# Kernel optimization log

Hardware: AMD Instinct MI355X
Metric: run time of the kernel (lower is better)

## Reference

```python
import jax, jax.numpy as jnp
import numpy as np

N, C = 50000, 91
K_PRE = 1000            # pre-NMS top-k candidates (fixed shape for jit)
DET_PER_IMG = 100
SCORE_THRESH = 0.05
NMS_THRESH = 0.5
MIN_SIZE = 0.01
LOG_SCALE_CLAMP = float(np.log(1000.0 / 16.0))  # torchvision BoxCoder clamp
BBOX_W = (10.0, 10.0, 5.0, 5.0)


def setup_inputs() -> dict:
    key = jax.random.key(0)
    k1, k2, k3, k4, k5, k6 = jax.random.split(key, 6)
    class_logits = jax.random.normal(k1, (N, C), jnp.float32) * 2.0
    box_regression = jax.random.normal(k2, (N, C * 4), jnp.float32) * 0.5
    x1 = jax.random.uniform(k3, (N,), jnp.float32) * 1200.0
    y1 = jax.random.uniform(k4, (N,), jnp.float32) * 700.0
    w = jax.random.uniform(k5, (N,), jnp.float32) * 150.0 + 4.0
    h = jax.random.uniform(k6, (N,), jnp.float32) * 150.0 + 4.0
    proposals = jnp.stack([x1, y1, x1 + w, y1 + h], axis=1)
    return {"class_logits": class_logits, "box_regression": box_regression,
            "proposals": proposals, "image_h": 800, "image_w": 1333}


def _decode(rel, props):
    # torchvision BoxCoder.decode_single with weights (10,10,5,5)
    wx, wy, ww, wh = BBOX_W
    pw = props[:, 2] - props[:, 0]
    ph = props[:, 3] - props[:, 1]
    cx = props[:, 0] + 0.5 * pw
    cy = props[:, 1] + 0.5 * ph
    dx = rel[:, 0] / wx
    dy = rel[:, 1] / wy
    dw = jnp.minimum(rel[:, 2] / ww, LOG_SCALE_CLAMP)
    dh = jnp.minimum(rel[:, 3] / wh, LOG_SCALE_CLAMP)
    pcx = dx * pw + cx
    pcy = dy * ph + cy
    ppw = jnp.exp(dw) * pw
    pph = jnp.exp(dh) * ph
    return jnp.stack([pcx - 0.5 * ppw, pcy - 0.5 * pph,
                      pcx + 0.5 * ppw, pcy + 0.5 * pph], axis=1)


def _iou_matrix(b):
    # b: [K,4] -> [K,K] pairwise IoU
    area = jnp.maximum(b[:, 2] - b[:, 0], 0.0) * jnp.maximum(b[:, 3] - b[:, 1], 0.0)
    lt = jnp.maximum(b[:, None, :2], b[None, :, :2])
    rb = jnp.minimum(b[:, None, 2:], b[None, :, 2:])
    wh = jnp.maximum(rb - lt, 0.0)
    inter = wh[..., 0] * wh[..., 1]
    return inter / (area[:, None] + area[None, :] - inter + 1e-7)


def _postprocess(class_logits, box_regression, proposals, image_h, image_w):
    num_classes = class_logits.shape[-1]
    n = proposals.shape[0]
    props = jnp.broadcast_to(proposals[:, None, :], (n, num_classes, 4)).reshape(-1, 4)
    boxes = _decode(box_regression.reshape(-1, 4), props)       # [N*C, 4]
    # clip_boxes_to_image
    boxes = jnp.stack([
        jnp.clip(boxes[:, 0], 0.0, float(image_w)),
        jnp.clip(boxes[:, 1], 0.0, float(image_h)),
        jnp.clip(boxes[:, 2], 0.0, float(image_w)),
        jnp.clip(boxes[:, 3], 0.0, float(image_h)),
    ], axis=1)
    scores = jax.nn.softmax(class_logits, axis=-1)               # [N, C]
    # drop background class 0
    boxes = boxes.reshape(n, num_classes, 4)[:, 1:].reshape(-1, 4)    # [N*(C-1), 4]
    scores = scores[:, 1:].reshape(-1)                                # [N*(C-1)]
    labels = jnp.broadcast_to(jnp.arange(1, num_classes), (n, num_classes - 1)).reshape(-1)
    # score threshold + remove small boxes -> mask (fixed-shape)
    w = boxes[:, 2] - boxes[:, 0]
    h = boxes[:, 3] - boxes[:, 1]
    valid = (scores > SCORE_THRESH) & (w >= MIN_SIZE) & (h >= MIN_SIZE)
    masked_scores = jnp.where(valid, scores, -1.0)
    s_k, idx = jax.lax.top_k(masked_scores, K_PRE)               # pre-NMS candidates
    b_k = boxes[idx]
    l_k = labels[idx]
    keep0 = s_k > 0.0
    # batched NMS via per-class coordinate offset
    offset = l_k.astype(b_k.dtype) * float(image_w + image_h + 2)
    iou = _iou_matrix(b_k + offset[:, None])                     # [K,K]
    ar = jnp.arange(K_PRE)
    def body(i, keep):
        sup = keep[i] & (iou[i] > NMS_THRESH) & (ar > i)
        return keep & ~sup
    keep = jax.lax.fori_loop(0, K_PRE, body, keep0)
    final_scores = jnp.where(keep, s_k, -1.0)
    s_out, j = jax.lax.top_k(final_scores, DET_PER_IMG)
    ok = s_out > 0.0
    boxes_out = jnp.where(ok[:, None], b_k[j], 0.0)
    scores_out = jnp.where(ok, s_out, 0.0)
    labels_out = jnp.where(ok, l_k[j], 0)
    return boxes_out, scores_out, labels_out


def reference(class_logits, box_regression, proposals, image_h, image_w):
    return _postprocess(class_logits, box_regression, proposals, image_h, image_w)
```

## Files before the change

### kernel.cpp

```cpp
#include <hip/hip_runtime.h>
#include <cstdint>

#define NROWS 50000
#define NCLS  91
#define KPRE  1000
#define NDET  100
#define CAP   4096
#define BIN_OFF 62770u
#define LOGCLAMP 4.135166556742356f
#define P1BLK 3125
#define R2BLK 49
#define NFINE 256
#define NU4   6250
#define CPS   3136
#define CP4   3528
#define GCHUNK 128

constexpr size_t OFF_CNT     = 0;
constexpr size_t OFF_ROWMAX  = 64;
constexpr size_t OFF_COMPACT = 100096;
constexpr size_t OFF_SSCORE  = 132864;
constexpr size_t OFF_SGIDX   = 136960;
constexpr size_t OFF_SLABEL  = 141056;
constexpr size_t OFF_BRAW    = 145152;
constexpr size_t OFF_BNMS    = 161536;
constexpr size_t OFF_MASK    = 177920;
constexpr size_t OFF_CPART   = 305920;

__device__ __forceinline__ bool decode_box(int row, int c,
    const float* __restrict__ regr, const float* __restrict__ props,
    float W, float H, float4& b) {
  const float4 rr = *reinterpret_cast<const float4*>(regr + (size_t)row * (NCLS * 4) + c * 4);
  const float4 pp = *reinterpret_cast<const float4*>(props + (size_t)row * 4);
  float pw = pp.z - pp.x, ph = pp.w - pp.y;
  float cx = pp.x + 0.5f * pw, cy = pp.y + 0.5f * ph;
  float dx = rr.x / 10.0f, dy = rr.y / 10.0f;
  float dw = fminf(rr.z / 5.0f, LOGCLAMP);
  float dh = fminf(rr.w / 5.0f, LOGCLAMP);
  float pcx = dx * pw + cx, pcy = dy * ph + cy;
  float ppw = expf(dw) * pw, pph = expf(dh) * ph;
  float x1 = fminf(fmaxf(pcx - 0.5f * ppw, 0.f), W);
  float y1 = fminf(fmaxf(pcy - 0.5f * pph, 0.f), H);
  float x2 = fminf(fmaxf(pcx + 0.5f * ppw, 0.f), W);
  float y2 = fminf(fmaxf(pcy + 0.5f * pph, 0.f), H);
  b = make_float4(x1, y1, x2, y2);
  return (x2 - x1 >= 0.01f) && (y2 - y1 >= 0.01f);
}

__device__ __forceinline__ bool decode_box_v(const float4& rr, const float4& pp,
                                             float W, float H, float4& b) {
  float pw = pp.z - pp.x, ph = pp.w - pp.y;
  float cx = pp.x + 0.5f * pw, cy = pp.y + 0.5f * ph;
  float dx = rr.x / 10.0f, dy = rr.y / 10.0f;
  float dw = fminf(rr.z / 5.0f, LOGCLAMP);
  float dh = fminf(rr.w / 5.0f, LOGCLAMP);
  float pcx = dx * pw + cx, pcy = dy * ph + cy;
  float ppw = expf(dw) * pw, pph = expf(dh) * ph;
  float x1 = fminf(fmaxf(pcx - 0.5f * ppw, 0.f), W);
  float y1 = fminf(fmaxf(pcy - 0.5f * pph, 0.f), H);
  float x2 = fminf(fmaxf(pcx + 0.5f * ppw, 0.f), W);
  float y2 = fminf(fmaxf(pcy + 0.5f * pph, 0.f), H);
  b = make_float4(x1, y1, x2, y2);
  return (x2 - x1 >= 0.01f) && (y2 - y1 >= 0.01f);
}

__global__ __launch_bounds__(256)
void pass1_kernel(const float* __restrict__ logits,
                  const float* __restrict__ regr,
                  const float* __restrict__ props,
                  const int* __restrict__ p_imh,
                  const int* __restrict__ p_imw,
                  uint16_t* __restrict__ rowmax,
                  uint16_t* __restrict__ cpart,
                  uint32_t* __restrict__ cnt) {
  __shared__ uint32_t lds9[9];
  const int t = threadIdx.x;
  if (blockIdx.x == 0 && t == 0) cnt[1] = 0;
  if (t < 9) lds9[t] = 0;
  __syncthreads();

  const int gt  = blockIdx.x * 256 + t;
  const int row = gt >> 4;
  const int sub = gt & 15;
  const float* lr = logits + (size_t)row * NCLS;
  const float4 pp = *reinterpret_cast<const float4*>(props + (size_t)row * 4);
  const float W = (float)(*p_imw), H = (float)(*p_imh);

  float x[6];
  #pragma unroll
  for (int j = 0; j < 6; ++j) {
    int c = sub + 16 * j;
    x[j] = (c < NCLS) ? lr[c] : -INFINITY;
  }
  float m = x[0];
  #pragma unroll
  for (int j = 1; j < 6; ++j) m = fmaxf(m, x[j]);
  m = fmaxf(m, __shfl_xor(m, 1));
  m = fmaxf(m, __shfl_xor(m, 2));
  m = fmaxf(m, __shfl_xor(m, 4));
  m = fmaxf(m, __shfl_xor(m, 8));
  float e[6]; float s = 0.f;
  #pragma unroll
  for (int j = 0; j < 6; ++j) {
    e[j] = (sub + 16 * j < NCLS) ? expf(x[j] - m) : 0.f;
    s += e[j];
  }
  s += __shfl_xor(s, 1);
  s += __shfl_xor(s, 2);
  s += __shfl_xor(s, 4);
  s += __shfl_xor(s, 8);

  const float4* rr4 = reinterpret_cast<const float4*>(regr) + (size_t)row * NCLS;
  float score[6]; bool ok[6]; float4 rrv[6];
  #pragma unroll
  for (int j = 0; j < 6; ++j) {
    int c = sub + 16 * j;
    score[j] = e[j] / s;
    ok[j] = (c >= 1) && (c < NCLS) && (score[j] > 0.05f);
    rrv[j] = ok[j] ? rr4[c] : make_float4(0.f, 0.f, 0.f, 0.f);
  }
  int maxbin = 0;
  #pragma unroll
  for (int j = 0; j < 6; ++j) {
    if (ok[j]) {
      float4 b;
      if (decode_box_v(rrv[j], pp, W, H, b)) {
        uint32_t bin = (__float_as_uint(score[j]) >> 14) - BIN_OFF;
        if ((int)bin > maxbin) maxbin = (int)bin;
      }
    }
  }
  maxbin = max(maxbin, __shfl_xor(maxbin, 1));
  maxbin = max(maxbin, __shfl_xor(maxbin, 2));
  maxbin = max(maxbin, __shfl_xor(maxbin, 4));
  maxbin = max(maxbin, __shfl_xor(maxbin, 8));
  if (sub == 0) {
    rowmax[row] = (uint16_t)maxbin;
    if (maxbin > 0) atomicAdd(&lds9[maxbin >> 8], 1u);
  }
  __syncthreads();
  if (t < 9) cpart[(size_t)t * CPS + blockIdx.x] = (uint16_t)lds9[t];
  if (blockIdx.x < 9 && t < CPS - P1BLK)
    cpart[(size_t)blockIdx.x * CPS + P1BLK + t] = 0;
}

__global__ __launch_bounds__(1024)
void refine_kernel(const float* __restrict__ logits,
                   const float* __restrict__ regr,
                   const float* __restrict__ props,
                   const int* __restrict__ p_imh,
                   const int* __restrict__ p_imw,
                   const uint16_t* __restrict__ rowmax,
                   const uint16_t* __restrict__ cpart,
                   uint32_t* __restrict__ cnt,
                   unsigned long long* __restrict__ compact) {
  __shared__ uint32_t fine[NFINE + 1];
  __shared__ uint32_t lds9[9];
  __shared__ uint32_t s_cut;
  const int t = threadIdx.x;
  if (t < 9) lds9[t] = 0;
  if (t < NFINE + 1) fine[t] = 0;
  if (t == 0) s_cut = 0xFFFFFFFFu;
  __syncthreads();

  const uint4* cp4 = reinterpret_cast<const uint4*>(cpart);
  for (int k = t; k < CP4; k += 1024) {
    uint4 v = cp4[k];
    uint32_t ssum = (v.x & 0xffffu) + (v.x >> 16) + (v.y & 0xffffu) + (v.y >> 16) +
                    (v.z & 0xffffu) + (v.z >> 16) + (v.w & 0xffffu) + (v.w >> 16);
    if (ssum) atomicAdd(&lds9[k / 392], ssum);
  }
  __syncthreads();
  uint32_t sfx[10];
  sfx[9] = 0;
  #pragma unroll
  for (int q = 8; q >= 0; --q) sfx[q] = sfx[q + 1] + lds9[q];
  const uint32_t total = sfx[0];
  uint32_t cut;
  if (total == 0) {
    cut = 0xFFFFFFFFu;
  } else {
    const uint32_t target = total < (uint32_t)KPRE ? total : (uint32_t)KPRE;
    int Bc = 0;
    uint32_t S_hi = 0;
    #pragma unroll
    for (int q = 8; q >= 0; --q) {
      if (sfx[q] >= target && sfx[q + 1] < target) { Bc = q; S_hi = sfx[q + 1]; }
    }
    const uint4* r128 = reinterpret_cast<const uint4*>(rowmax);
    for (int k = t; k < NU4; k += 1024) {
      uint4 v = r128[k];
      #pragma unroll
      for (int w = 0; w < 4; ++w) {
        uint32_t u = (w == 0) ? v.x : (w == 1) ? v.y : (w == 2) ? v.z : v.w;
        uint32_t a = u & 0xffffu, b = u >> 16;
        if (a && (a >> 8) == (uint32_t)Bc) atomicAdd(&fine[a & 255u], 1u);
        if (b && (b >> 8) == (uint32_t)Bc) atomicAdd(&fine[b & 255u], 1u);
      }
    }
    __syncthreads();
    for (int off = 1; off < NFINE; off <<= 1) {
      uint32_t add = (t < NFINE && t + off < NFINE) ? fine[t + off] : 0;
      __syncthreads();
      if (t < NFINE) fine[t] += add;
      __syncthreads();
    }
    if (t < NFINE) {
      uint32_t hi = S_hi + fine[t];
      uint32_t hin = S_hi + ((t < NFINE - 1) ? fine[t + 1] : 0);
      if (hi >= target && hin < target) s_cut = ((uint32_t)Bc << 8) + (uint32_t)t;
    }
    __syncthreads();
    cut = s_cut;
  }

  const int lane = t & 63;
  const int g16 = lane >> 4;
  const int sub = lane & 15;
  const float W = (float)(*p_imw), H = (float)(*p_imh);
  const int base = blockIdx.x * 1024;
  const int myrow0 = base + t;
  bool qual = (myrow0 < NROWS) && ((uint32_t)rowmax[myrow0] >= cut);
  unsigned long long bm = __ballot(qual);
  if (!bm) return;
  const int waveBase = base + (t & ~63);
  while (bm) {
    int bsel[4];
    #pragma unroll
    for (int k = 0; k < 4; ++k) {
      bsel[k] = bm ? (__ffsll((unsigned long long)bm) - 1) : -1;
      if (bm) bm &= bm - 1;
    }
    const int myb = bsel[g16];
    const int row = waveBase + (myb >= 0 ? myb : 0);
    const float* lr = logits + (size_t)row * NCLS;
    float x[6];
    #pragma unroll
    for (int j = 0; j < 6; ++j) {
      int c = sub + 16 * j;
      x[j] = (c < NCLS) ? lr[c] : -INFINITY;
    }
    float m = x[0];
    #pragma unroll
    for (int j = 1; j < 6; ++j) m = fmaxf(m, x[j]);
    m = fmaxf(m, __shfl_xor(m, 1));
    m = fmaxf(m, __shfl_xor(m, 2));
    m = fmaxf(m, __shfl_xor(m, 4));
    m = fmaxf(m, __shfl_xor(m, 8));
    float e[6]; float s = 0.f;
    #pragma unroll
    for (int j = 0; j < 6; ++j) {
      e[j] = (sub + 16 * j < NCLS) ? expf(x[j] - m) : 0.f;
      s += e[j];
    }
    s += __shfl_xor(s, 1);
    s += __shfl_xor(s, 2);
    s += __shfl_xor(s, 4);
    s += __shfl_xor(s, 8);
    if (myb >= 0) {
      #pragma unroll
      for (int j = 0; j < 6; ++j) {
        int c = sub + 16 * j;
        if (c >= 1 && c < NCLS) {
          float score = e[j] / s;
          if (score > 0.05f) {
            float4 bb;
            if (decode_box(row, c, regr, props, W, H, bb)) {
              uint32_t bits = __float_as_uint(score);
              uint32_t bin = (bits >> 14) - BIN_OFF;
              if (bin >= cut) {
                uint32_t pos = atomicAdd(&cnt[1], 1u);
                if (pos < CAP) {
                  uint32_t gidx = (uint32_t)row * 90u + (uint32_t)(c - 1);
                  compact[pos] = ((unsigned long long)bits << 32) |
                                 (unsigned long long)(0xFFFFFFFFu - gidx);
                }
              }
            }
          }
        }
      }
    }
  }
}

__global__ __launch_bounds__(1024)
void sort_prep_kernel(const unsigned long long* __restrict__ compact,
                      const uint32_t* __restrict__ cnt,
                      const float* __restrict__ regr, const float* __restrict__ props,
                      const int* __restrict__ p_imh, const int* __restrict__ p_imw,
                      float* __restrict__ sel_score, uint32_t* __restrict__ sel_gidx,
                      int* __restrict__ slabel, float4* __restrict__ braw,
                      float4* __restrict__ bnms) {
  __shared__ unsigned long long arr[CAP];
  const int t = threadIdx.x;
  const uint32_t M = cnt[1] < (uint32_t)CAP ? cnt[1] : (uint32_t)CAP;
  int P = 1024;
  while (P < (int)M) P <<= 1;
  for (int i = t; i < P; i += 1024) arr[i] = (i < (int)M) ? compact[i] : 0ull;
  __syncthreads();
  for (int k = 2; k <= P; k <<= 1) {
    for (int j = k >> 1; j > 0; j >>= 1) {
      for (int i = t; i < P; i += 1024) {
        int l = i ^ j;
        if (l > i) {
          unsigned long long A = arr[i], B = arr[l];
          bool up = ((i & k) == 0);
          if (up ? (A > B) : (A < B)) { arr[i] = B; arr[l] = A; }
        }
      }
      __syncthreads();
    }
  }
  if (t < KPRE) {
    unsigned long long en = arr[P - 1 - t];
    float sc; uint32_t g;
    if (en) { sc = __uint_as_float((uint32_t)(en >> 32)); g = 0xFFFFFFFFu - (uint32_t)en; }
    else    { sc = -1.f; g = 0xFFFFFFFFu; }
    sel_score[t] = sc;
    sel_gidx[t] = g;
    if (sc > 0.f) {
      int row = (int)(g / 90u);
      int c   = (int)(g % 90u) + 1;
      float W = (float)(*p_imw), H = (float)(*p_imh);
      float4 b;
      decode_box(row, c, regr, props, W, H, b);
      braw[t] = b;
      float offv = (float)c * (float)(*p_imw + *p_imh + 2);
      bnms[t] = make_float4(b.x + offv, b.y + offv, b.z + offv, b.w + offv);
      slabel[t] = c;
    } else {
      braw[t] = make_float4(0, 0, 0, 0);
      bnms[t] = make_float4(0, 0, 0, 0);
      slabel[t] = 0;
    }
  }
}

__global__ __launch_bounds__(256)
void iou_kernel(const float4* __restrict__ bnms, unsigned long long* __restrict__ mask) {
  const int i = blockIdx.x;
  const int lane = threadIdx.x & 63;
  const int wv = threadIdx.x >> 6;
  const float4 bi = bnms[i];
  const float areai = fmaxf(bi.z - bi.x, 0.f) * fmaxf(bi.w - bi.y, 0.f);
  #pragma unroll
  for (int ww = 0; ww < 4; ++ww) {
    int wd = wv * 4 + ww;
    int j = wd * 64 + lane;
    bool bit = false;
    if (j < KPRE && j > i) {
      float4 bj = bnms[j];
      float areaj = fmaxf(bj.z - bj.x, 0.f) * fmaxf(bj.w - bj.y, 0.f);
      float ltx = fmaxf(bi.x, bj.x), lty = fmaxf(bi.y, bj.y);
      float rbx = fminf(bi.z, bj.z), rby = fminf(bi.w, bj.w);
      float iw = fmaxf(rbx - ltx, 0.f), ih = fmaxf(rby - lty, 0.f);
      float inter = iw * ih;
      float iou = inter / (areai + areaj - inter + 1e-7f);
      bit = iou > 0.5f;
    }
    unsigned long long mword = __ballot(bit);
    if (lane == 0) mask[(size_t)i * 16 + wd] = mword;
  }
}

__global__ __launch_bounds__(256)
void greedy_kernel(const unsigned long long* __restrict__ mask,
                   const float* __restrict__ sel_score,
                   const int* __restrict__ slabel,
                   const float4* __restrict__ braw,
                   float* __restrict__ out) {
  __shared__ ulonglong2 buf[2][GCHUNK * 8];
  __shared__ int kept[NDET];
  __shared__ int s_done;
  const int t = threadIdx.x;
  const int lane = t & 63;
  const int wv = t >> 6;
  const ulonglong2* gm2 = reinterpret_cast<const ulonglong2*>(mask);
  constexpr int NCHUNK = (KPRE + GCHUNK - 1) / GCHUNK;

  unsigned long long kw = 0ull;
  #pragma unroll
  for (int w = 0; w < 16; ++w) {
    int j = w * 64 + lane;
    bool b = (j < KPRE) && (sel_score[j] > 0.f);
    unsigned long long mword = __ballot(b);
    if (lane == w) kw = mword;
  }
  if (t == 0) s_done = 0;

  {
    int rows = (KPRE < GCHUNK) ? KPRE : GCHUNK;
    int n2 = rows * 8;
    for (int k = t; k < n2; k += 256) buf[0][k] = gm2[k];
  }
  __syncthreads();

  int kc = 0;
  for (int c = 0; c < NCHUNK; ++c) {
    if (wv > 0 && c + 1 < NCHUNK) {
      int rows = KPRE - (c + 1) * GCHUNK;
      if (rows > GCHUNK) rows = GCHUNK;
      int n2 = rows * 8;
      size_t gbase = (size_t)(c + 1) * GCHUNK * 8;
      for (int k = t - 64; k < n2; k += 192) buf[(c + 1) & 1][k] = gm2[gbase + k];
    }
    if (wv == 0) {
      const unsigned long long* bb =
          reinterpret_cast<const unsigned long long*>(buf[c & 1]);
      int rows = KPRE - c * GCHUNK;
      if (rows > GCHUNK) rows = GCHUNK;
      unsigned long long curm = (lane < 16) ? bb[lane] : 0ull;
      for (int r = 0; r < rows; ++r) {
        unsigned long long nxt =
            (lane < 16 && r + 1 < rows) ? bb[(r + 1) * 16 + lane] : 0ull;
        int i = c * GCHUNK + r;
        unsigned long long kwv = __shfl(kw, i >> 6);
        if ((kwv >> (i & 63)) & 1ull) {
          if (lane == 0) kept[kc] = i;
          kw &= ~curm;
          ++kc;
          if (kc >= NDET) { if (lane == 0) s_done = 1; break; }
        }
        curm = nxt;
      }
    }
    __syncthreads();
    if (s_done) break;
  }

  if (wv == 0) {
    for (int q = lane; q < NDET; q += 64) {
      if (q < kc) {
        int i = kept[q];
        float4 b = braw[i];
        out[q * 4 + 0] = b.x; out[q * 4 + 1] = b.y;
        out[q * 4 + 2] = b.z; out[q * 4 + 3] = b.w;
        out[4 * NDET + q] = sel_score[i];
        out[5 * NDET + q] = (float)slabel[i];
      } else {
        out[q * 4 + 0] = 0.f; out[q * 4 + 1] = 0.f;
        out[q * 4 + 2] = 0.f; out[q * 4 + 3] = 0.f;
        out[4 * NDET + q] = 0.f;
        out[5 * NDET + q] = 0.f;
      }
    }
  }
}

extern "C" void kernel_launch(void* const* d_in, const int* in_sizes, int n_in,
                              void* d_out, int out_size, void* d_ws, size_t ws_size,
                              hipStream_t stream) {
  const float* logits = (const float*)d_in[0];
  const float* regr   = (const float*)d_in[1];
  const float* props  = (const float*)d_in[2];
  const int*   p_imh  = (const int*)d_in[3];
  const int*   p_imw  = (const int*)d_in[4];
  float* out = (float*)d_out;

  uint8_t* ws = (uint8_t*)d_ws;
  uint32_t* cnt  = (uint32_t*)(ws + OFF_CNT);
  uint16_t* rowmax = (uint16_t*)(ws + OFF_ROWMAX);
  unsigned long long* compact = (unsigned long long*)(ws + OFF_COMPACT);
  float*    sel_score = (float*)(ws + OFF_SSCORE);
  uint32_t* sel_gidx  = (uint32_t*)(ws + OFF_SGIDX);
  int*      slabel    = (int*)(ws + OFF_SLABEL);
  float4*   braw      = (float4*)(ws + OFF_BRAW);
  float4*   bnms      = (float4*)(ws + OFF_BNMS);
  unsigned long long* mask = (unsigned long long*)(ws + OFF_MASK);
  uint16_t* cpart     = (uint16_t*)(ws + OFF_CPART);

  pass1_kernel<<<P1BLK, 256, 0, stream>>>(
      logits, regr, props, p_imh, p_imw, rowmax, cpart, cnt);
  refine_kernel<<<R2BLK, 1024, 0, stream>>>(
      logits, regr, props, p_imh, p_imw, rowmax, cpart, cnt, compact);
  sort_prep_kernel<<<1, 1024, 0, stream>>>(compact, cnt, regr, props, p_imh, p_imw,
                                           sel_score, sel_gidx, slabel, braw, bnms);
  iou_kernel<<<KPRE, 256, 0, stream>>>(bnms, mask);
  greedy_kernel<<<1, 256, 0, stream>>>(mask, sel_score, slabel, braw, out);
}
```

Before: 90.01 us.

## Fuse sort into refine and greedy NMS into IoU via last-block-done pattern

The single-block sort/prep kernel is folded into the refine kernel, and the greedy NMS kernel is folded into the IoU kernel. In each case an atomic counter elects the last finishing block, which then runs the serial stage. This cuts two kernel launches and their inter-kernel gaps from the five-launch pipeline. In exchange, refine blocks now reserve 32KB of shared memory for the sort array, which may lower occupancy, and correctness now depends on threadfence ordering.

Result: slower. 161.4 us (+79.4%).

```diff
diff --git a/kernel.cpp b/kernel.cpp
--- a/kernel.cpp
+++ b/kernel.cpp
@@ -75,7 +75,7 @@
                   uint32_t* __restrict__ cnt) {
   __shared__ uint32_t lds9[9];
   const int t = threadIdx.x;
-  if (blockIdx.x == 0 && t == 0) cnt[1] = 0;
+  if (blockIdx.x == 0 && t == 0) { cnt[1] = 0; cnt[2] = 0; cnt[3] = 0; }
   if (t < 9) lds9[t] = 0;
   __syncthreads();
 
@@ -153,10 +153,15 @@
                    const uint16_t* __restrict__ rowmax,
                    const uint16_t* __restrict__ cpart,
                    uint32_t* __restrict__ cnt,
-                   unsigned long long* __restrict__ compact) {
+                   unsigned long long* __restrict__ compact,
+                   float* __restrict__ sel_score, uint32_t* __restrict__ sel_gidx,
+                   int* __restrict__ slabel, float4* __restrict__ braw,
+                   float4* __restrict__ bnms) {
+  __shared__ unsigned long long arr[CAP];
   __shared__ uint32_t fine[NFINE + 1];
   __shared__ uint32_t lds9[9];
   __shared__ uint32_t s_cut;
+  __shared__ uint32_t s_prev;
   const int t = threadIdx.x;
   if (t < 9) lds9[t] = 0;
   if (t < NFINE + 1) fine[t] = 0;
@@ -214,66 +219,67 @@
     cut = s_cut;
   }
 
-  const int lane = t & 63;
-  const int g16 = lane >> 4;
-  const int sub = lane & 15;
-  const float W = (float)(*p_imw), H = (float)(*p_imh);
-  const int base = blockIdx.x * 1024;
-  const int myrow0 = base + t;
-  bool qual = (myrow0 < NROWS) && ((uint32_t)rowmax[myrow0] >= cut);
-  unsigned long long bm = __ballot(qual);
-  if (!bm) return;
-  const int waveBase = base + (t & ~63);
-  while (bm) {
-    int bsel[4];
-    #pragma unroll
-    for (int k = 0; k < 4; ++k) {
-      bsel[k] = bm ? (__ffsll((unsigned long long)bm) - 1) : -1;
-      if (bm) bm &= bm - 1;
-    }
-    const int myb = bsel[g16];
-    const int row = waveBase + (myb >= 0 ? myb : 0);
-    const float* lr = logits + (size_t)row * NCLS;
-    float x[6];
-    #pragma unroll
-    for (int j = 0; j < 6; ++j) {
-      int c = sub + 16 * j;
-      x[j] = (c < NCLS) ? lr[c] : -INFINITY;
-    }
-    float m = x[0];
-    #pragma unroll
-    for (int j = 1; j < 6; ++j) m = fmaxf(m, x[j]);
-    m = fmaxf(m, __shfl_xor(m, 1));
-    m = fmaxf(m, __shfl_xor(m, 2));
-    m = fmaxf(m, __shfl_xor(m, 4));
-    m = fmaxf(m, __shfl_xor(m, 8));
-    float e[6]; float s = 0.f;
-    #pragma unroll
-    for (int j = 0; j < 6; ++j) {
-      e[j] = (sub + 16 * j < NCLS) ? expf(x[j] - m) : 0.f;
-      s += e[j];
-    }
-    s += __shfl_xor(s, 1);
-    s += __shfl_xor(s, 2);
-    s += __shfl_xor(s, 4);
-    s += __shfl_xor(s, 8);
-    if (myb >= 0) {
+  {
+    const int lane = t & 63;
+    const int g16 = lane >> 4;
+    const int sub = lane & 15;
+    const float W = (float)(*p_imw), H = (float)(*p_imh);
+    const int base = blockIdx.x * 1024;
+    const int myrow0 = base + t;
+    bool qual = (myrow0 < NROWS) && ((uint32_t)rowmax[myrow0] >= cut);
+    unsigned long long bm = __ballot(qual);
+    const int waveBase = base + (t & ~63);
+    while (bm) {
+      int bsel[4];
+      #pragma unroll
+      for (int k = 0; k < 4; ++k) {
+        bsel[k] = bm ? (__ffsll((unsigned long long)bm) - 1) : -1;
+        if (bm) bm &= bm - 1;
+      }
+      const int myb = bsel[g16];
+      const int row = waveBase + (myb >= 0 ? myb : 0);
+      const float* lr = logits + (size_t)row * NCLS;
+      float x[6];
       #pragma unroll
       for (int j = 0; j < 6; ++j) {
         int c = sub + 16 * j;
-        if (c >= 1 && c < NCLS) {
-          float score = e[j] / s;
-          if (score > 0.05f) {
-            float4 bb;
-            if (decode_box(row, c, regr, props, W, H, bb)) {
-              uint32_t bits = __float_as_uint(score);
-              uint32_t bin = (bits >> 14) - BIN_OFF;
-              if (bin >= cut) {
-                uint32_t pos = atomicAdd(&cnt[1], 1u);
-                if (pos < CAP) {
-                  uint32_t gidx = (uint32_t)row * 90u + (uint32_t)(c - 1);
-                  compact[pos] = ((unsigned long long)bits << 32) |
-                                 (unsigned long long)(0xFFFFFFFFu - gidx);
+        x[j] = (c < NCLS) ? lr[c] : -INFINITY;
+      }
+      float m = x[0];
+      #pragma unroll
+      for (int j = 1; j < 6; ++j) m = fmaxf(m, x[j]);
+      m = fmaxf(m, __shfl_xor(m, 1));
+      m = fmaxf(m, __shfl_xor(m, 2));
+      m = fmaxf(m, __shfl_xor(m, 4));
+      m = fmaxf(m, __shfl_xor(m, 8));
+      float e[6]; float s = 0.f;
+      #pragma unroll
+      for (int j = 0; j < 6; ++j) {
+        e[j] = (sub + 16 * j < NCLS) ? expf(x[j] - m) : 0.f;
+        s += e[j];
+      }
+      s += __shfl_xor(s, 1);
+      s += __shfl_xor(s, 2);
+      s += __shfl_xor(s, 4);
+      s += __shfl_xor(s, 8);
+      if (myb >= 0) {
+        #pragma unroll
+        for (int j = 0; j < 6; ++j) {
+          int c = sub + 16 * j;
+          if (c >= 1 && c < NCLS) {
+            float score = e[j] / s;
+            if (score > 0.05f) {
+              float4 bb;
+              if (decode_box(row, c, regr, props, W, H, bb)) {
+                uint32_t bits = __float_as_uint(score);
+                uint32_t bin = (bits >> 14) - BIN_OFF;
+                if (bin >= cut) {
+                  uint32_t pos = atomicAdd(&cnt[1], 1u);
+                  if (pos < CAP) {
+                    uint32_t gidx = (uint32_t)row * 90u + (uint32_t)(c - 1);
+                    compact[pos] = ((unsigned long long)bits << 32) |
+                                   (unsigned long long)(0xFFFFFFFFu - gidx);
+                  }
                 }
               }
             }
@@ -282,18 +288,14 @@
       }
     }
   }
-}
-
-__global__ __launch_bounds__(1024)
-void sort_prep_kernel(const unsigned long long* __restrict__ compact,
-                      const uint32_t* __restrict__ cnt,
-                      const float* __restrict__ regr, const float* __restrict__ props,
-                      const int* __restrict__ p_imh, const int* __restrict__ p_imw,
-                      float* __restrict__ sel_score, uint32_t* __restrict__ sel_gidx,
-                      int* __restrict__ slabel, float4* __restrict__ braw,
-                      float4* __restrict__ bnms) {
-  __shared__ unsigned long long arr[CAP];
-  const int t = threadIdx.x;
+
+  __syncthreads();
+  __threadfence();
+  if (t == 0) s_prev = atomicAdd(&cnt[2], 1u);
+  __syncthreads();
+  if (s_prev != (uint32_t)(R2BLK - 1)) return;
+  __threadfence();
+
   const uint32_t M = cnt[1] < (uint32_t)CAP ? cnt[1] : (uint32_t)CAP;
   int P = 1024;
   while (P < (int)M) P <<= 1;
@@ -338,44 +340,50 @@
 }
 
 __global__ __launch_bounds__(256)
-void iou_kernel(const float4* __restrict__ bnms, unsigned long long* __restrict__ mask) {
-  const int i = blockIdx.x;
-  const int lane = threadIdx.x & 63;
-  const int wv = threadIdx.x >> 6;
-  const float4 bi = bnms[i];
-  const float areai = fmaxf(bi.z - bi.x, 0.f) * fmaxf(bi.w - bi.y, 0.f);
-  #pragma unroll
-  for (int ww = 0; ww < 4; ++ww) {
-    int wd = wv * 4 + ww;
-    int j = wd * 64 + lane;
-    bool bit = false;
-    if (j < KPRE && j > i) {
-      float4 bj = bnms[j];
-      float areaj = fmaxf(bj.z - bj.x, 0.f) * fmaxf(bj.w - bj.y, 0.f);
-      float ltx = fmaxf(bi.x, bj.x), lty = fmaxf(bi.y, bj.y);
-      float rbx = fminf(bi.z, bj.z), rby = fminf(bi.w, bj.w);
-      float iw = fmaxf(rbx - ltx, 0.f), ih = fmaxf(rby - lty, 0.f);
-      float inter = iw * ih;
-      float iou = inter / (areai + areaj - inter + 1e-7f);
-      bit = iou > 0.5f;
-    }
-    unsigned long long mword = __ballot(bit);
-    if (lane == 0) mask[(size_t)i * 16 + wd] = mword;
-  }
-}
-
-__global__ __launch_bounds__(256)
-void greedy_kernel(const unsigned long long* __restrict__ mask,
-                   const float* __restrict__ sel_score,
-                   const int* __restrict__ slabel,
-                   const float4* __restrict__ braw,
-                   float* __restrict__ out) {
+void iou_kernel(const float4* __restrict__ bnms, unsigned long long* __restrict__ mask,
+                const float* __restrict__ sel_score,
+                const int* __restrict__ slabel,
+                const float4* __restrict__ braw,
+                uint32_t* __restrict__ cnt,
+                float* __restrict__ out) {
   __shared__ ulonglong2 buf[2][GCHUNK * 8];
   __shared__ int kept[NDET];
   __shared__ int s_done;
+  __shared__ uint32_t s_prev;
+  const int i = blockIdx.x;
   const int t = threadIdx.x;
   const int lane = t & 63;
   const int wv = t >> 6;
+  {
+    const float4 bi = bnms[i];
+    const float areai = fmaxf(bi.z - bi.x, 0.f) * fmaxf(bi.w - bi.y, 0.f);
+    #pragma unroll
+    for (int ww = 0; ww < 4; ++ww) {
+      int wd = wv * 4 + ww;
+      int j = wd * 64 + lane;
+      bool bit = false;
+      if (j < KPRE && j > i) {
+        float4 bj = bnms[j];
+        float areaj = fmaxf(bj.z - bj.x, 0.f) * fmaxf(bj.w - bj.y, 0.f);
+        float ltx = fmaxf(bi.x, bj.x), lty = fmaxf(bi.y, bj.y);
+        float rbx = fminf(bi.z, bj.z), rby = fminf(bi.w, bj.w);
+        float iw = fmaxf(rbx - ltx, 0.f), ih = fmaxf(rby - lty, 0.f);
+        float inter = iw * ih;
+        float iou = inter / (areai + areaj - inter + 1e-7f);
+        bit = iou > 0.5f;
+      }
+      unsigned long long mword = __ballot(bit);
+      if (lane == 0) mask[(size_t)i * 16 + wd] = mword;
+    }
+  }
+
+  __syncthreads();
+  __threadfence();
+  if (t == 0) s_prev = atomicAdd(&cnt[3], 1u);
+  __syncthreads();
+  if (s_prev != (uint32_t)(KPRE - 1)) return;
+  __threadfence();
+
   const ulonglong2* gm2 = reinterpret_cast<const ulonglong2*>(mask);
   constexpr int NCHUNK = (KPRE + GCHUNK - 1) / GCHUNK;
 
@@ -414,10 +422,10 @@
       for (int r = 0; r < rows; ++r) {
         unsigned long long nxt =
             (lane < 16 && r + 1 < rows) ? bb[(r + 1) * 16 + lane] : 0ull;
-        int i = c * GCHUNK + r;
-        unsigned long long kwv = __shfl(kw, i >> 6);
-        if ((kwv >> (i & 63)) & 1ull) {
-          if (lane == 0) kept[kc] = i;
+        int ii = c * GCHUNK + r;
+        unsigned long long kwv = __shfl(kw, ii >> 6);
+        if ((kwv >> (ii & 63)) & 1ull) {
+          if (lane == 0) kept[kc] = ii;
           kw &= ~curm;
           ++kc;
           if (kc >= NDET) { if (lane == 0) s_done = 1; break; }
@@ -432,12 +440,12 @@
   if (wv == 0) {
     for (int q = lane; q < NDET; q += 64) {
       if (q < kc) {
-        int i = kept[q];
-        float4 b = braw[i];
+        int ii = kept[q];
+        float4 b = braw[ii];
         out[q * 4 + 0] = b.x; out[q * 4 + 1] = b.y;
         out[q * 4 + 2] = b.z; out[q * 4 + 3] = b.w;
-        out[4 * NDET + q] = sel_score[i];
-        out[5 * NDET + q] = (float)slabel[i];
+        out[4 * NDET + q] = sel_score[ii];
+        out[5 * NDET + q] = (float)slabel[ii];
       } else {
         out[q * 4 + 0] = 0.f; out[q * 4 + 1] = 0.f;
         out[q * 4 + 2] = 0.f; out[q * 4 + 3] = 0.f;
@@ -473,9 +481,8 @@
   pass1_kernel<<<P1BLK, 256, 0, stream>>>(
       logits, regr, props, p_imh, p_imw, rowmax, cpart, cnt);
   refine_kernel<<<R2BLK, 1024, 0, stream>>>(
-      logits, regr, props, p_imh, p_imw, rowmax, cpart, cnt, compact);
-  sort_prep_kernel<<<1, 1024, 0, stream>>>(compact, cnt, regr, props, p_imh, p_imw,
-                                           sel_score, sel_gidx, slabel, braw, bnms);
-  iou_kernel<<<KPRE, 256, 0, stream>>>(bnms, mask);
-  greedy_kernel<<<1, 256, 0, stream>>>(mask, sel_score, slabel, braw, out);
-}
+      logits, regr, props, p_imh, p_imw, rowmax, cpart, cnt, compact,
+      sel_score, sel_gidx, slabel, braw, bnms);
+  iou_kernel<<<KPRE, 256, 0, stream>>>(
+      bnms, mask, sel_score, slabel, braw, cnt, out);
+}
```

## Replace bitonic sort with rank counting and fuse IoU with greedy NMS

Applied to the files above, without the earlier changes.

The single-block bitonic sort of the compacted candidates is replaced by a rank-by-counting pass. Each thread compares its up to four keys against all M keys in LDS and scatters the top-K entries, decoding boxes as it goes. The IoU mask kernel and the greedy NMS kernel become one launch of 50 blocks, each computing 20 mask rows. The last block to finish, found through an atomic counter, runs the greedy pass. This removes one kernel launch and many barrier-separated sort stages, at the cost of O(M^2) comparisons and a last-block-done handoff that depends on threadfence ordering.

Measured after the change: 161.2 us. +79.2%, slower.

```diff
diff --git a/kernel.cpp b/kernel.cpp
--- a/kernel.cpp
+++ b/kernel.cpp
@@ -15,6 +15,8 @@
 #define CPS   3136
 #define CP4   3528
 #define GCHUNK 128
+#define IRPB  20
+#define IBLK  50
 
 constexpr size_t OFF_CNT     = 0;
 constexpr size_t OFF_ROWMAX  = 64;
@@ -75,7 +77,7 @@
                   uint32_t* __restrict__ cnt) {
   __shared__ uint32_t lds9[9];
   const int t = threadIdx.x;
-  if (blockIdx.x == 0 && t == 0) cnt[1] = 0;
+  if (blockIdx.x == 0 && t == 0) { cnt[1] = 0; cnt[2] = 0; }
   if (t < 9) lds9[t] = 0;
   __syncthreads();
 
@@ -285,97 +287,109 @@
 }
 
 __global__ __launch_bounds__(1024)
-void sort_prep_kernel(const unsigned long long* __restrict__ compact,
+void rank_prep_kernel(const unsigned long long* __restrict__ compact,
                       const uint32_t* __restrict__ cnt,
                       const float* __restrict__ regr, const float* __restrict__ props,
                       const int* __restrict__ p_imh, const int* __restrict__ p_imw,
                       float* __restrict__ sel_score, uint32_t* __restrict__ sel_gidx,
                       int* __restrict__ slabel, float4* __restrict__ braw,
                       float4* __restrict__ bnms) {
-  __shared__ unsigned long long arr[CAP];
+  __shared__ unsigned long long keys[CAP];
   const int t = threadIdx.x;
-  const uint32_t M = cnt[1] < (uint32_t)CAP ? cnt[1] : (uint32_t)CAP;
-  int P = 1024;
-  while (P < (int)M) P <<= 1;
-  for (int i = t; i < P; i += 1024) arr[i] = (i < (int)M) ? compact[i] : 0ull;
-  __syncthreads();
-  for (int k = 2; k <= P; k <<= 1) {
-    for (int j = k >> 1; j > 0; j >>= 1) {
-      for (int i = t; i < P; i += 1024) {
-        int l = i ^ j;
-        if (l > i) {
-          unsigned long long A = arr[i], B = arr[l];
-          bool up = ((i & k) == 0);
-          if (up ? (A > B) : (A < B)) { arr[i] = B; arr[l] = A; }
-        }
-      }
-      __syncthreads();
-    }
-  }
-  if (t < KPRE) {
-    unsigned long long en = arr[P - 1 - t];
-    float sc; uint32_t g;
-    if (en) { sc = __uint_as_float((uint32_t)(en >> 32)); g = 0xFFFFFFFFu - (uint32_t)en; }
-    else    { sc = -1.f; g = 0xFFFFFFFFu; }
-    sel_score[t] = sc;
-    sel_gidx[t] = g;
-    if (sc > 0.f) {
+  const int M = (int)(cnt[1] < (uint32_t)CAP ? cnt[1] : (uint32_t)CAP);
+  for (int i = t; i < M; i += 1024) keys[i] = compact[i];
+  __syncthreads();
+
+  const int i0 = t, i1 = t + 1024, i2 = t + 2048, i3 = t + 3072;
+  const unsigned long long K_INV = 0xFFFFFFFFFFFFFFFFull;
+  unsigned long long k0 = (i0 < M) ? keys[i0] : K_INV;
+  unsigned long long k1 = (i1 < M) ? keys[i1] : K_INV;
+  unsigned long long k2 = (i2 < M) ? keys[i2] : K_INV;
+  unsigned long long k3 = (i3 < M) ? keys[i3] : K_INV;
+  int r0 = 0, r1 = 0, r2 = 0, r3 = 0;
+  for (int j = 0; j < M; ++j) {
+    unsigned long long kj = keys[j];
+    r0 += (kj > k0); r1 += (kj > k1); r2 += (kj > k2); r3 += (kj > k3);
+  }
+
+  const float W = (float)(*p_imw), H = (float)(*p_imh);
+  const float offmul = (float)(*p_imw + *p_imh + 2);
+  #pragma unroll
+  for (int q = 0; q < 4; ++q) {
+    const int ii = (q == 0) ? i0 : (q == 1) ? i1 : (q == 2) ? i2 : i3;
+    const unsigned long long kk = (q == 0) ? k0 : (q == 1) ? k1 : (q == 2) ? k2 : k3;
+    const int rr = (q == 0) ? r0 : (q == 1) ? r1 : (q == 2) ? r2 : r3;
+    if (ii < M && rr < KPRE) {
+      float sc = __uint_as_float((uint32_t)(kk >> 32));
+      uint32_t g = 0xFFFFFFFFu - (uint32_t)kk;
+      sel_score[rr] = sc;
+      sel_gidx[rr] = g;
       int row = (int)(g / 90u);
       int c   = (int)(g % 90u) + 1;
-      float W = (float)(*p_imw), H = (float)(*p_imh);
       float4 b;
       decode_box(row, c, regr, props, W, H, b);
-      braw[t] = b;
-      float offv = (float)c * (float)(*p_imw + *p_imh + 2);
-      bnms[t] = make_float4(b.x + offv, b.y + offv, b.z + offv, b.w + offv);
-      slabel[t] = c;
-    } else {
-      braw[t] = make_float4(0, 0, 0, 0);
-      bnms[t] = make_float4(0, 0, 0, 0);
-      slabel[t] = 0;
-    }
+      braw[rr] = b;
+      float offv = (float)c * offmul;
+      bnms[rr] = make_float4(b.x + offv, b.y + offv, b.z + offv, b.w + offv);
+      slabel[rr] = c;
+    }
+  }
+  if (t >= M && t < KPRE) {
+    sel_score[t] = -1.f;
+    sel_gidx[t] = 0xFFFFFFFFu;
+    braw[t] = make_float4(0, 0, 0, 0);
+    bnms[t] = make_float4(0, 0, 0, 0);
+    slabel[t] = 0;
   }
 }
 
 __global__ __launch_bounds__(256)
-void iou_kernel(const float4* __restrict__ bnms, unsigned long long* __restrict__ mask) {
-  const int i = blockIdx.x;
-  const int lane = threadIdx.x & 63;
-  const int wv = threadIdx.x >> 6;
-  const float4 bi = bnms[i];
-  const float areai = fmaxf(bi.z - bi.x, 0.f) * fmaxf(bi.w - bi.y, 0.f);
-  #pragma unroll
-  for (int ww = 0; ww < 4; ++ww) {
-    int wd = wv * 4 + ww;
-    int j = wd * 64 + lane;
-    bool bit = false;
-    if (j < KPRE && j > i) {
-      float4 bj = bnms[j];
-      float areaj = fmaxf(bj.z - bj.x, 0.f) * fmaxf(bj.w - bj.y, 0.f);
-      float ltx = fmaxf(bi.x, bj.x), lty = fmaxf(bi.y, bj.y);
-      float rbx = fminf(bi.z, bj.z), rby = fminf(bi.w, bj.w);
-      float iw = fmaxf(rbx - ltx, 0.f), ih = fmaxf(rby - lty, 0.f);
-      float inter = iw * ih;
-      float iou = inter / (areai + areaj - inter + 1e-7f);
-      bit = iou > 0.5f;
-    }
-    unsigned long long mword = __ballot(bit);
-    if (lane == 0) mask[(size_t)i * 16 + wd] = mword;
-  }
-}
-
-__global__ __launch_bounds__(256)
-void greedy_kernel(const unsigned long long* __restrict__ mask,
-                   const float* __restrict__ sel_score,
-                   const int* __restrict__ slabel,
-                   const float4* __restrict__ braw,
-                   float* __restrict__ out) {
+void iou_greedy_kernel(const float4* __restrict__ bnms,
+                       unsigned long long* __restrict__ mask,
+                       const float* __restrict__ sel_score,
+                       const int* __restrict__ slabel,
+                       const float4* __restrict__ braw,
+                       uint32_t* __restrict__ cnt,
+                       float* __restrict__ out) {
   __shared__ ulonglong2 buf[2][GCHUNK * 8];
   __shared__ int kept[NDET];
   __shared__ int s_done;
+  __shared__ uint32_t s_prev;
   const int t = threadIdx.x;
   const int lane = t & 63;
   const int wv = t >> 6;
+
+  const int r0 = blockIdx.x * IRPB;
+  for (int i = r0; i < r0 + IRPB && i < KPRE; ++i) {
+    const float4 bi = bnms[i];
+    const float areai = fmaxf(bi.z - bi.x, 0.f) * fmaxf(bi.w - bi.y, 0.f);
+    #pragma unroll
+    for (int ww = 0; ww < 4; ++ww) {
+      int wd = wv * 4 + ww;
+      int j = wd * 64 + lane;
+      bool bit = false;
+      if (j < KPRE && j > i) {
+        float4 bj = bnms[j];
+        float areaj = fmaxf(bj.z - bj.x, 0.f) * fmaxf(bj.w - bj.y, 0.f);
+        float ltx = fmaxf(bi.x, bj.x), lty = fmaxf(bi.y, bj.y);
+        float rbx = fminf(bi.z, bj.z), rby = fminf(bi.w, bj.w);
+        float iw = fmaxf(rbx - ltx, 0.f), ih = fmaxf(rby - lty, 0.f);
+        float inter = iw * ih;
+        float iou = inter / (areai + areaj - inter + 1e-7f);
+        bit = iou > 0.5f;
+      }
+      unsigned long long mword = __ballot(bit);
+      if (lane == 0) mask[(size_t)i * 16 + wd] = mword;
+    }
+  }
+
+  __syncthreads();
+  __threadfence();
+  if (t == 0) s_prev = atomicAdd(&cnt[2], 1u);
+  __syncthreads();
+  if (s_prev != (uint32_t)(IBLK - 1)) return;
+  __threadfence();
+
   const ulonglong2* gm2 = reinterpret_cast<const ulonglong2*>(mask);
   constexpr int NCHUNK = (KPRE + GCHUNK - 1) / GCHUNK;
 
@@ -474,8 +488,8 @@
       logits, regr, props, p_imh, p_imw, rowmax, cpart, cnt);
   refine_kernel<<<R2BLK, 1024, 0, stream>>>(
       logits, regr, props, p_imh, p_imw, rowmax, cpart, cnt, compact);
-  sort_prep_kernel<<<1, 1024, 0, stream>>>(compact, cnt, regr, props, p_imh, p_imw,
+  rank_prep_kernel<<<1, 1024, 0, stream>>>(compact, cnt, regr, props, p_imh, p_imw,
                                            sel_score, sel_gidx, slabel, braw, bnms);
-  iou_kernel<<<KPRE, 256, 0, stream>>>(bnms, mask);
-  greedy_kernel<<<1, 256, 0, stream>>>(mask, sel_score, slabel, braw, out);
-}
+  iou_greedy_kernel<<<IBLK, 256, 0, stream>>>(
+      bnms, mask, sel_score, slabel, braw, cnt, out);
+}
```

## Replace single-block bitonic sort with multi-block rank-by-counting selection

Applied to the files above, without the earlier changes.

The single-block shared-memory bitonic sort of up to 4096 candidate keys is replaced by a rank computation. Each thread counts how many keys exceed its own key and, if its rank is below KPRE, writes its decoded box directly to that slot. The work is spread over 4 blocks and drops the many __syncthreads stages of the bitonic network, at the cost of O(M^2) shared-memory comparisons. Keys are unique because the candidate index is packed into the low bits, so ranks do not collide.

New measurement: 93.47 us. +3.8%, slower.

```diff
diff --git a/kernel.cpp b/kernel.cpp
--- a/kernel.cpp
+++ b/kernel.cpp
@@ -15,6 +15,7 @@
 #define CPS   3136
 #define CP4   3528
 #define GCHUNK 128
+#define RNKB  4
 
 constexpr size_t OFF_CNT     = 0;
 constexpr size_t OFF_ROWMAX  = 64;
@@ -285,55 +286,55 @@
 }
 
 __global__ __launch_bounds__(1024)
-void sort_prep_kernel(const unsigned long long* __restrict__ compact,
+void rank_prep_kernel(const unsigned long long* __restrict__ compact,
                       const uint32_t* __restrict__ cnt,
                       const float* __restrict__ regr, const float* __restrict__ props,
                       const int* __restrict__ p_imh, const int* __restrict__ p_imw,
                       float* __restrict__ sel_score, uint32_t* __restrict__ sel_gidx,
                       int* __restrict__ slabel, float4* __restrict__ braw,
                       float4* __restrict__ bnms) {
-  __shared__ unsigned long long arr[CAP];
+  __shared__ unsigned long long keys[CAP];
   const int t = threadIdx.x;
-  const uint32_t M = cnt[1] < (uint32_t)CAP ? cnt[1] : (uint32_t)CAP;
-  int P = 1024;
-  while (P < (int)M) P <<= 1;
-  for (int i = t; i < P; i += 1024) arr[i] = (i < (int)M) ? compact[i] : 0ull;
-  __syncthreads();
-  for (int k = 2; k <= P; k <<= 1) {
-    for (int j = k >> 1; j > 0; j >>= 1) {
-      for (int i = t; i < P; i += 1024) {
-        int l = i ^ j;
-        if (l > i) {
-          unsigned long long A = arr[i], B = arr[l];
-          bool up = ((i & k) == 0);
-          if (up ? (A > B) : (A < B)) { arr[i] = B; arr[l] = A; }
-        }
-      }
-      __syncthreads();
-    }
-  }
-  if (t < KPRE) {
-    unsigned long long en = arr[P - 1 - t];
-    float sc; uint32_t g;
-    if (en) { sc = __uint_as_float((uint32_t)(en >> 32)); g = 0xFFFFFFFFu - (uint32_t)en; }
-    else    { sc = -1.f; g = 0xFFFFFFFFu; }
-    sel_score[t] = sc;
-    sel_gidx[t] = g;
-    if (sc > 0.f) {
-      int row = (int)(g / 90u);
-      int c   = (int)(g % 90u) + 1;
-      float W = (float)(*p_imw), H = (float)(*p_imh);
-      float4 b;
-      decode_box(row, c, regr, props, W, H, b);
-      braw[t] = b;
-      float offv = (float)c * (float)(*p_imw + *p_imh + 2);
-      bnms[t] = make_float4(b.x + offv, b.y + offv, b.z + offv, b.w + offv);
-      slabel[t] = c;
-    } else {
-      braw[t] = make_float4(0, 0, 0, 0);
-      bnms[t] = make_float4(0, 0, 0, 0);
-      slabel[t] = 0;
-    }
+  const int M = (int)(cnt[1] < (uint32_t)CAP ? cnt[1] : (uint32_t)CAP);
+  for (int i = t; i < M; i += 1024) keys[i] = compact[i];
+  __syncthreads();
+
+  const int ii = blockIdx.x * 1024 + t;
+  const unsigned long long kk = (ii < M) ? keys[ii] : 0xFFFFFFFFFFFFFFFFull;
+  int r = 0;
+  int j = 0;
+  const int M16 = M & ~15;
+  #pragma unroll 1
+  for (; j < M16; j += 16) {
+    int acc = 0;
+    #pragma unroll
+    for (int u = 0; u < 16; ++u) acc += (keys[j + u] > kk);
+    r += acc;
+  }
+  for (; j < M; ++j) r += (keys[j] > kk);
+
+  const float W = (float)(*p_imw), H = (float)(*p_imh);
+  const float offmul = (float)(*p_imw + *p_imh + 2);
+  if (ii < M && r < KPRE) {
+    float sc = __uint_as_float((uint32_t)(kk >> 32));
+    uint32_t g = 0xFFFFFFFFu - (uint32_t)kk;
+    sel_score[r] = sc;
+    sel_gidx[r] = g;
+    int row = (int)(g / 90u);
+    int c   = (int)(g % 90u) + 1;
+    float4 b;
+    decode_box(row, c, regr, props, W, H, b);
+    braw[r] = b;
+    float offv = (float)c * offmul;
+    bnms[r] = make_float4(b.x + offv, b.y + offv, b.z + offv, b.w + offv);
+    slabel[r] = c;
+  }
+  if (blockIdx.x == 0 && t >= M && t < KPRE) {
+    sel_score[t] = -1.f;
+    sel_gidx[t] = 0xFFFFFFFFu;
+    braw[t] = make_float4(0, 0, 0, 0);
+    bnms[t] = make_float4(0, 0, 0, 0);
+    slabel[t] = 0;
   }
 }
 
@@ -474,8 +475,8 @@
       logits, regr, props, p_imh, p_imw, rowmax, cpart, cnt);
   refine_kernel<<<R2BLK, 1024, 0, stream>>>(
       logits, regr, props, p_imh, p_imw, rowmax, cpart, cnt, compact);
-  sort_prep_kernel<<<1, 1024, 0, stream>>>(compact, cnt, regr, props, p_imh, p_imw,
-                                           sel_score, sel_gidx, slabel, braw, bnms);
+  rank_prep_kernel<<<RNKB, 1024, 0, stream>>>(compact, cnt, regr, props, p_imh, p_imw,
+                                              sel_score, sel_gidx, slabel, braw, bnms);
   iou_kernel<<<KPRE, 256, 0, stream>>>(bnms, mask);
   greedy_kernel<<<1, 256, 0, stream>>>(mask, sel_score, slabel, braw, out);
 }
```
